# Kernel optimization log

Measured on AMD Instinct MI355X. Metric: run time of the kernel, lower is better.

The kernel has to match this reference:

```python
import jax, jax.numpy as jnp
import numpy as np

N = 50000      # nodes
E = 800000     # edges (avg degree 16)
IN = 128       # in_feats
HID = 32       # hidden_feats per head
H = 4          # num_heads
NEG_SLOPE = 0.2


def setup_inputs() -> dict:
    key = jax.random.key(0)
    ks = jax.random.split(key, 13)
    x = jax.random.normal(ks[0], (N, IN), jnp.float32)
    src = jax.random.randint(ks[1], (E,), 0, N, jnp.int32)
    dst = jax.random.randint(ks[2], (E,), 0, N, jnp.int32)

    def lin(k, fi, fo):
        return jax.random.normal(k, (fi, fo), jnp.float32) * (1.0 / np.sqrt(fi))

    # conv1: IN -> H*HID
    W1 = lin(ks[3], IN, H * HID)
    al1 = jax.random.normal(ks[4], (H, HID), jnp.float32) * 0.1
    ar1 = jax.random.normal(ks[5], (H, HID), jnp.float32) * 0.1
    b1 = jnp.zeros((H, HID), jnp.float32)
    # conv2: H*HID -> H*HID
    W2 = lin(ks[6], H * HID, H * HID)
    al2 = jax.random.normal(ks[7], (H, HID), jnp.float32) * 0.1
    ar2 = jax.random.normal(ks[8], (H, HID), jnp.float32) * 0.1
    b2 = jnp.zeros((H, HID), jnp.float32)
    # fc: HID -> 1
    fcW = lin(ks[9], HID, 1)
    fcb = jnp.zeros((1,), jnp.float32)
    return {"x": x, "src": src, "dst": dst,
            "W1": W1, "al1": al1, "ar1": ar1, "b1": b1,
            "W2": W2, "al2": al2, "ar2": ar2, "b2": b2,
            "fcW": fcW, "fcb": fcb}


def gat_conv(x, src, dst, W, al, ar, b):
    # x: [N, F_in] -> feat: [N, H, HID]
    feat = (x @ W).reshape(N, H, HID)
    el = jnp.sum(feat * al, axis=-1)            # [N, H]
    er = jnp.sum(feat * ar, axis=-1)            # [N, H]
    e = jax.nn.leaky_relu(el[src] + er[dst], NEG_SLOPE)  # [E, H]
    # segment softmax over incoming edges of each dst node
    m = jax.ops.segment_max(e, dst, num_segments=N)      # [N, H]
    ex = jnp.exp(e - m[dst])                              # [E, H]
    denom = jax.ops.segment_sum(ex, dst, num_segments=N)  # [N, H]
    alpha = ex / denom[dst]                                # [E, H]
    msg = feat[src] * alpha[:, :, None]                    # [E, H, HID]
    out = jax.ops.segment_sum(msg, dst, num_segments=N)   # [N, H, HID]
    return out + b[None, :, :]


def reference(x, src, dst, W1, al1, ar1, b1, W2, al2, ar2, b2, fcW, fcb):
    h = gat_conv(x, src, dst, W1, al1, ar1, b1).reshape(N, H * HID)
    h = jax.nn.relu(h)
    # dropout(0.5) is identity in eval mode
    h = gat_conv(h, src, dst, W2, al2, ar2, b2).mean(axis=1)  # [N, HID]
    return h @ fcW + fcb                                       # [N, 1]
```

## Files before the change

### kernel.cpp

```cpp
#include <hip/hip_runtime.h>
#include <hip/hip_fp16.h>

#define LEAK 0.2f
#define CAP 64
#define CS 16

static __device__ inline int swz(int c, int j) {
    int qb = j >> 3, r = j & 7;
    return c * 144 + qb * 8 + (qb >> 2) * 4 + r;
}
static __device__ inline unsigned q4(float4 v, float is) {
    int x0 = __float2int_rn(v.x * is) + 128; x0 = min(max(x0, 0), 255);
    int x1 = __float2int_rn(v.y * is) + 128; x1 = min(max(x1, 0), 255);
    int x2 = __float2int_rn(v.z * is) + 128; x2 = min(max(x2, 0), 255);
    int x3 = __float2int_rn(v.w * is) + 128; x3 = min(max(x3, 0), 255);
    return (unsigned)x0 | ((unsigned)x1 << 8) | ((unsigned)x2 << 16) | ((unsigned)x3 << 24);
}

__global__ __launch_bounds__(256, 4) void k1(
    const float* __restrict__ X, const float* __restrict__ W,
    const float* __restrict__ al, const float* __restrict__ ar,
    float2* __restrict__ elsc2, float* __restrict__ er_nh,
    unsigned* __restrict__ fq8,
    int* __restrict__ cnt,
    const float* __restrict__ W2, const float* __restrict__ al2,
    const float* __restrict__ ar2, const float* __restrict__ fcW,
    const float* __restrict__ b2, float* __restrict__ WfT,
    float* __restrict__ bc, int N, int ntiles, int zb) {
    __shared__ float sW[32 * 128];
    __shared__ float sXT[32 * 128];
    const int b = blockIdx.x;
    const int t = threadIdx.x;

    if (b >= ntiles) {
        int bb = b - ntiles;
        if (bb < zb) {
            int i = bb * 256 + t;
            if (i < N * (CS / 4)) {
                ((int4*)cnt)[i] = make_int4(0, 0, 0, 0);
            }
        } else {
            int idx = (bb - zb) * 256 + t;
            if (idx < 1536) {
                int c = idx >> 7, k = idx & 127;
                int h = c & 3, sel = c >> 2;
                const float* vec = (sel == 0) ? (al2 + 32 * h)
                                 : (sel == 1) ? (ar2 + 32 * h) : fcW;
                float s = 0.f;
#pragma unroll 8
                for (int m = 0; m < 32; m++) s += W2[k * 128 + 32 * h + m] * vec[m];
                WfT[c * 128 + k] = s;
            } else if (idx < 1540) {
                int h = idx - 1536;
                float s = 0.f;
                for (int m = 0; m < 32; m++) s += b2[h * 32 + m] * fcW[m];
                bc[h] = s;
            }
        }
        return;
    }

    const int r0 = b * 128;
    const int tx = t & 15;
    const int ty = t >> 4;
    const float4* X4 = (const float4*)X;
    const float4* W4 = (const float4*)W;
    float4* sW4 = (float4*)sW;
    const float4* sXT4 = (const float4*)sXT;

    float4 acc[8][2];
#pragma unroll
    for (int r = 0; r < 8; r++) {
        acc[r][0] = make_float4(0.f, 0.f, 0.f, 0.f);
        acc[r][1] = make_float4(0.f, 0.f, 0.f, 0.f);
    }
    for (int ks = 0; ks < 4; ++ks) {
        if (ks) __syncthreads();
#pragma unroll
        for (int i = 0; i < 4; i++) {
            int idx = i * 256 + t;
            sW4[idx] = W4[1024 * ks + idx];
        }
#pragma unroll
        for (int i = 0; i < 4; i++) {
            int idx = i * 256 + t;
            int row = idx >> 3;
            int kq = idx & 7;
            float4 v = make_float4(0.f, 0.f, 0.f, 0.f);
            if (r0 + row < N) v = X4[(size_t)(r0 + row) * 32 + ks * 8 + kq];
            int sc = (((row >> 2) ^ kq)) * 4 + (row & 3);
            sXT[(4 * kq + 0) * 128 + sc] = v.x;
            sXT[(4 * kq + 1) * 128 + sc] = v.y;
            sXT[(4 * kq + 2) * 128 + sc] = v.z;
            sXT[(4 * kq + 3) * 128 + sc] = v.w;
        }
        __syncthreads();
#pragma unroll 4
        for (int k = 0; k < 32; k++) {
            float4 w0 = sW4[k * 32 + tx];
            float4 w1 = sW4[k * 32 + 16 + tx];
            float4 x0 = sXT4[k * 32 + (ty ^ (k >> 2))];
            float4 x1 = sXT4[k * 32 + ((16 + ty) ^ (k >> 2))];
            float xs[8] = {x0.x, x0.y, x0.z, x0.w, x1.x, x1.y, x1.z, x1.w};
#pragma unroll
            for (int r = 0; r < 8; r++) {
                acc[r][0].x += xs[r] * w0.x; acc[r][0].y += xs[r] * w0.y;
                acc[r][0].z += xs[r] * w0.z; acc[r][0].w += xs[r] * w0.w;
                acc[r][1].x += xs[r] * w1.x; acc[r][1].y += xs[r] * w1.y;
                acc[r][1].z += xs[r] * w1.z; acc[r][1].w += xs[r] * w1.w;
            }
        }
    }
    const float4* al4p = (const float4*)al;
    const float4* ar4p = (const float4*)ar;
    float4 alA = al4p[tx], alB = al4p[16 + tx];
    float4 arA = ar4p[tx], arB = ar4p[16 + tx];
#pragma unroll
    for (int r = 0; r < 8; r++) {
        int lrow = (r < 4) ? (ty * 4 + r) : (64 + ty * 4 + (r - 4));
        int row = r0 + lrow;
        bool ok = row < N;
        float4 a0 = acc[r][0], a1 = acc[r][1];
        float m = fmaxf(fmaxf(fmaxf(fabsf(a0.x), fabsf(a0.y)),
                              fmaxf(fabsf(a0.z), fabsf(a0.w))),
                        fmaxf(fmaxf(fabsf(a1.x), fabsf(a1.y)),
                              fmaxf(fabsf(a1.z), fabsf(a1.w))));
#pragma unroll
        for (int off = 1; off < 16; off <<= 1) m = fmaxf(m, __shfl_xor(m, off));
        float scale = m * (1.f / 127.f);
        float is = (m > 0.f) ? (127.f / m) : 0.f;
        if (ok) {
            fq8[(size_t)row * 32 + tx] = q4(a0, is);
            fq8[(size_t)row * 32 + 16 + tx] = q4(a1, is);
        }
        float elA = a0.x * alA.x + a0.y * alA.y + a0.z * alA.z + a0.w * alA.w;
        float erA = a0.x * arA.x + a0.y * arA.y + a0.z * arA.z + a0.w * arA.w;
        float elB = a1.x * alB.x + a1.y * alB.y + a1.z * alB.z + a1.w * alB.w;
        float erB = a1.x * arB.x + a1.y * arB.y + a1.z * arB.z + a1.w * arB.w;
#pragma unroll
        for (int off = 1; off < 8; off <<= 1) {
            elA += __shfl_xor(elA, off); erA += __shfl_xor(erA, off);
            elB += __shfl_xor(elB, off); erB += __shfl_xor(erB, off);
        }
        if (ok && tx == 0) {
            elsc2[row * 4 + 0] = make_float2(elA, scale);
            elsc2[row * 4 + 2] = make_float2(elB, scale);
            er_nh[row * 4 + 0] = erA;
            er_nh[row * 4 + 2] = erB;
        }
        if (ok && tx == 8) {
            elsc2[row * 4 + 1] = make_float2(elA, scale);
            elsc2[row * 4 + 3] = make_float2(elB, scale);
            er_nh[row * 4 + 1] = erA;
            er_nh[row * 4 + 3] = erB;
        }
    }
}

__global__ __launch_bounds__(256) void k_ell(
    const int* __restrict__ src, const int* __restrict__ dst,
    int* __restrict__ cnt, unsigned short* __restrict__ ell,
    int E, int N, int R) {
    const int part = blockIdx.x & 7;
    const int rank = blockIdx.x >> 3;
    const int S = (N + 7) >> 3;
    const int lo = part * S;
    const int hi = (lo + S < N) ? (lo + S) : N;
    const int per = (E + R - 1) / R;
    const int e0 = rank * per;
    const int e1 = (e0 + per < E) ? (e0 + per) : E;
    for (int e = e0 + threadIdx.x; e < e1; e += 256) {
        int d = dst[e];
        if (d >= lo && d < hi) {
            int s = src[e];
            int pos = atomicAdd(&cnt[d * CS], 1);
            if (pos < CAP) ell[(size_t)d * CAP + pos] = (unsigned short)s;
        }
    }
}

__global__ __launch_bounds__(256) void k_agg1P(
    const unsigned* __restrict__ fq8, const float2* __restrict__ elsc2,
    const float* __restrict__ er_nh, const unsigned short* __restrict__ ell,
    const int* __restrict__ cnt, const float* __restrict__ b1,
    const float* __restrict__ WfT, float2* __restrict__ Pag,
    float* __restrict__ er2, int N) {
    __shared__ float sWf[12 * 144];
    for (int i = threadIdx.x; i < 1536; i += 256)
        sWf[swz(i >> 7, i & 127)] = WfT[i];
    __syncthreads();
    const int wave = threadIdx.x >> 6, lane = threadIdx.x & 63;
    const int nsub = lane >> 4, q = lane & 15, h = q >> 2;
    const int wbase = q * 8 + (q >> 2) * 4;
    const uint2* fq2 = (const uint2*)fq8;

    const int n = blockIdx.x * 16 + wave * 4 + nsub;
    const bool nok = n < N;
    const int nc = nok ? n : (N - 1);
    int deg = nok ? cnt[n * CS] : 0; if (deg > CAP) deg = CAP;
    float er = nok ? er_nh[n * 4 + h] : 0.f;
    const unsigned short* row = ell + (size_t)nc * CAP;

    int dm = deg;
    dm = max(dm, __shfl_xor(dm, 16));
    dm = max(dm, __shfl_xor(dm, 32));

    float acc[8] = {0.f, 0.f, 0.f, 0.f, 0.f, 0.f, 0.f, 0.f};
    float den = 0.f, wss = 0.f;
    for (int jt = 0; jt < dm; jt += 16) {
        int s_all = (jt + q < CAP) ? (int)row[jt + q] : 0;
        int lim = dm - jt; if (lim > 16) lim = 16;
        for (int u = 0; u < lim; u += 8) {
            int sv[8]; float2 esv[8]; uint2 fv[8];
#pragma unroll
            for (int v = 0; v < 8; v++) {
                int jj = jt + u + v;
                int s = __shfl(s_all, (lane & 48) | ((u + v) & 15));
                sv[v] = (jj < deg) ? s : 0;
            }
#pragma unroll
            for (int v = 0; v < 8; v++) esv[v] = elsc2[sv[v] * 4 + h];
#pragma unroll
            for (int v = 0; v < 8; v++) fv[v] = fq2[(size_t)sv[v] * 16 + q];
#pragma unroll
            for (int v = 0; v < 8; v++) {
                int jj = jt + u + v;
                bool valid = jj < deg;
                float e = esv[v].x + er;
                e = fmaxf(e, LEAK * e);
                float w = valid ? __expf(e) : 0.f;
                float ws = w * esv[v].y;
                unsigned ua = fv[v].x, ub = fv[v].y;
                acc[0] += ws * (float)(ua & 0xff);
                acc[1] += ws * (float)((ua >> 8) & 0xff);
                acc[2] += ws * (float)((ua >> 16) & 0xff);
                acc[3] += ws * (float)(ua >> 24);
                acc[4] += ws * (float)(ub & 0xff);
                acc[5] += ws * (float)((ub >> 8) & 0xff);
                acc[6] += ws * (float)((ub >> 16) & 0xff);
                acc[7] += ws * (float)(ub >> 24);
                den += w; wss += ws;
            }
        }
    }
    float inv = (den > 0.f) ? (1.f / den) : 0.f;
    float off128 = 128.f * wss;
    float4 b1a = ((const float4*)b1)[q * 2];
    float4 b1b = ((const float4*)b1)[q * 2 + 1];
    float hv[8];
    hv[0] = fmaxf((acc[0] - off128) * inv + b1a.x, 0.f);
    hv[1] = fmaxf((acc[1] - off128) * inv + b1a.y, 0.f);
    hv[2] = fmaxf((acc[2] - off128) * inv + b1a.z, 0.f);
    hv[3] = fmaxf((acc[3] - off128) * inv + b1a.w, 0.f);
    hv[4] = fmaxf((acc[4] - off128) * inv + b1b.x, 0.f);
    hv[5] = fmaxf((acc[5] - off128) * inv + b1b.y, 0.f);
    hv[6] = fmaxf((acc[6] - off128) * inv + b1b.z, 0.f);
    hv[7] = fmaxf((acc[7] - off128) * inv + b1b.w, 0.f);
    float p[12];
#pragma unroll
    for (int c = 0; c < 12; c++) {
        const float* wr = sWf + c * 144 + wbase;
        float4 wa = *(const float4*)wr;
        float4 wb = *(const float4*)(wr + 4);
        p[c] = hv[0] * wa.x + hv[1] * wa.y + hv[2] * wa.z + hv[3] * wa.w
             + hv[4] * wb.x + hv[5] * wb.y + hv[6] * wb.z + hv[7] * wb.w;
    }
#pragma unroll
    for (int off = 1; off < 16; off <<= 1) {
#pragma unroll
        for (int c = 0; c < 12; c++) p[c] += __shfl_xor(p[c], off);
    }
    if (nok) {
        if (q < 4) Pag[(size_t)n * 4 + q] = make_float2(p[q], p[8 + q]);
        else if (q < 8) er2[(size_t)n * 4 + (q - 4)] = p[q];
    }
}

__global__ __launch_bounds__(256) void k_agg2(
    const float2* __restrict__ Pag, const float* __restrict__ er2,
    const unsigned short* __restrict__ ell, const int* __restrict__ cnt,
    const float* __restrict__ bc, const float* __restrict__ fcb,
    float* __restrict__ out, int N) {
    int idx = blockIdx.x * 256 + threadIdx.x;
    int n = idx >> 2, h = idx & 3;
    if (n >= N) return;
    int deg = cnt[n * CS]; if (deg > CAP) deg = CAP;
    float er = er2[(size_t)n * 4 + h];
    const unsigned short* row = ell + (size_t)n * CAP;
    float num = 0.f, den = 0.f;
    int j = 0, d8 = deg & ~7;
    for (; j < d8; j += 8) {
        ushort4 sa = *(const ushort4*)(row + j);
        ushort4 sb = *(const ushort4*)(row + j + 4);
        int sv[8] = {sa.x, sa.y, sa.z, sa.w, sb.x, sb.y, sb.z, sb.w};
        float2 g[8];
#pragma unroll
        for (int v = 0; v < 8; v++) g[v] = Pag[(size_t)sv[v] * 4 + h];
#pragma unroll
        for (int v = 0; v < 8; v++) {
            float e = g[v].x + er; e = fmaxf(e, LEAK * e);
            float w = __expf(e);
            num += w * g[v].y; den += w;
        }
    }
    for (; j < deg; ++j) {
        int s = row[j];
        float2 gg = Pag[(size_t)s * 4 + h];
        float e = gg.x + er; e = fmaxf(e, LEAK * e);
        float w = __expf(e);
        num += w * gg.y; den += w;
    }
    float r = (den > 0.f) ? (num / den) : 0.f;
    r += bc[h];
    r += __shfl_xor(r, 1);
    r += __shfl_xor(r, 2);
    if (h == 0) out[n] = 0.25f * r + fcb[0];
}

extern "C" void kernel_launch(void* const* d_in, const int* in_sizes, int n_in,
                              void* d_out, int out_size, void* d_ws, size_t ws_size,
                              hipStream_t stream) {
    const float* x   = (const float*)d_in[0];
    const int* src   = (const int*)d_in[1];
    const int* dst   = (const int*)d_in[2];
    const float* W1  = (const float*)d_in[3];
    const float* al1 = (const float*)d_in[4];
    const float* ar1 = (const float*)d_in[5];
    const float* b1  = (const float*)d_in[6];
    const float* W2  = (const float*)d_in[7];
    const float* al2 = (const float*)d_in[8];
    const float* ar2 = (const float*)d_in[9];
    const float* b2  = (const float*)d_in[10];
    const float* fcW = (const float*)d_in[11];
    const float* fcb = (const float*)d_in[12];
    float* out = (float*)d_out;

    const int N = in_sizes[0] / 128;
    const int E = in_sizes[1];

    char* w = (char*)d_ws;
    size_t off = 0;
    auto alloc = [&](size_t bytes) {
        void* p = w + off;
        off = (off + bytes + 255) & ~(size_t)255;
        return p;
    };
    unsigned* fq8  = (unsigned*)alloc((size_t)N * 32 * 4);
    float2* elsc2  = (float2*)alloc((size_t)N * 4 * 8);
    float* er_nh   = (float*)alloc((size_t)N * 4 * 4);
    float2* Pag    = (float2*)alloc((size_t)N * 4 * 8);
    float* er2     = (float*)alloc((size_t)N * 4 * 4);
    float* WfT     = (float*)alloc((size_t)(12 * 128 + 4) * 4);
    float* bc      = WfT + 12 * 128;
    int* cnt       = (int*)alloc((size_t)N * CS * 4);
    unsigned short* ell = (unsigned short*)alloc((size_t)N * CAP * 2);

    const int zb = (N * (CS / 4) + 255) / 256;
    const int ntiles = (N + 127) / 128;
    const int R = 256;

    k1<<<ntiles + zb + 8, 256, 0, stream>>>(
        x, W1, al1, ar1, elsc2, er_nh, fq8,
        cnt, W2, al2, ar2, fcW, b2, WfT, bc, N, ntiles, zb);
    k_ell<<<8 * R, 256, 0, stream>>>(src, dst, cnt, ell, E, N, R);
    k_agg1P<<<(N + 15) / 16, 256, 0, stream>>>(
        fq8, elsc2, er_nh, ell, cnt, b1, WfT, Pag, er2, N);
    k_agg2<<<(N * 4 + 255) / 256, 256, 0, stream>>>(
        Pag, er2, ell, cnt, bc, fcb, out, N);
}
```

Baseline: 200.5 us.

## Fuse ELL build into GEMM kernel and move init work to separate kernel

Moves the cnt zeroing and the W2/fcW folding into a new small kernel k0. The ELL-construction blocks are merged into the first-layer GEMM kernel as extra blocks so edge bucketing runs concurrently with the feature projection. The GEMM tile shrinks from 128 to 64 rows per block, halving accumulators and shared memory, which gives more blocks to mix with the atomic-heavy ELL blocks. The cost is an extra launch for k0 and less register-level reuse per GEMM block.

```diff
diff --git a/kernel.cpp b/kernel.cpp
--- a/kernel.cpp
+++ b/kernel.cpp
@@ -17,50 +17,72 @@
     return (unsigned)x0 | ((unsigned)x1 << 8) | ((unsigned)x2 << 16) | ((unsigned)x3 << 24);
 }
 
-__global__ __launch_bounds__(256, 4) void k1(
+__global__ __launch_bounds__(256) void k0(
+    int* __restrict__ cnt,
+    const float* __restrict__ W2, const float* __restrict__ al2,
+    const float* __restrict__ ar2, const float* __restrict__ fcW,
+    const float* __restrict__ b2, float* __restrict__ WfT,
+    float* __restrict__ bc, int N, int zb) {
+    const int b = blockIdx.x;
+    const int t = threadIdx.x;
+    if (b < zb) {
+        int i = b * 256 + t;
+        if (i < N * (CS / 4)) ((int4*)cnt)[i] = make_int4(0, 0, 0, 0);
+        return;
+    }
+    int idx = (b - zb) * 256 + t;
+    if (idx < 1536) {
+        int c = idx >> 7, k = idx & 127;
+        int h = c & 3, sel = c >> 2;
+        const float* vec = (sel == 0) ? (al2 + 32 * h)
+                         : (sel == 1) ? (ar2 + 32 * h) : fcW;
+        float s = 0.f;
+#pragma unroll 8
+        for (int m = 0; m < 32; m++) s += W2[k * 128 + 32 * h + m] * vec[m];
+        WfT[c * 128 + k] = s;
+    } else if (idx < 1540) {
+        int h = idx - 1536;
+        float s = 0.f;
+        for (int m = 0; m < 32; m++) s += b2[h * 32 + m] * fcW[m];
+        bc[h] = s;
+    }
+}
+
+__global__ __launch_bounds__(256, 4) void k1f(
     const float* __restrict__ X, const float* __restrict__ W,
     const float* __restrict__ al, const float* __restrict__ ar,
     float2* __restrict__ elsc2, float* __restrict__ er_nh,
     unsigned* __restrict__ fq8,
-    int* __restrict__ cnt,
-    const float* __restrict__ W2, const float* __restrict__ al2,
-    const float* __restrict__ ar2, const float* __restrict__ fcW,
-    const float* __restrict__ b2, float* __restrict__ WfT,
-    float* __restrict__ bc, int N, int ntiles, int zb) {
+    const int* __restrict__ src, const int* __restrict__ dst,
+    int* __restrict__ cnt, unsigned short* __restrict__ ell,
+    int N, int E, int gtiles, int R) {
     __shared__ float sW[32 * 128];
-    __shared__ float sXT[32 * 128];
+    __shared__ float sXT[32 * 64];
     const int b = blockIdx.x;
     const int t = threadIdx.x;
 
-    if (b >= ntiles) {
-        int bb = b - ntiles;
-        if (bb < zb) {
-            int i = bb * 256 + t;
-            if (i < N * (CS / 4)) {
-                ((int4*)cnt)[i] = make_int4(0, 0, 0, 0);
+    if (b >= gtiles) {
+        const int bb = b - gtiles;
+        const int part = bb & 7;
+        const int rank = bb >> 3;
+        const int S = (N + 7) >> 3;
+        const int lo = part * S;
+        const int hi = (lo + S < N) ? (lo + S) : N;
+        const int per = (E + R - 1) / R;
+        const int e0 = rank * per;
+        const int e1 = (e0 + per < E) ? (e0 + per) : E;
+        for (int e = e0 + t; e < e1; e += 256) {
+            int d = dst[e];
+            if (d >= lo && d < hi) {
+                int s = src[e];
+                int pos = atomicAdd(&cnt[d * CS], 1);
+                if (pos < CAP) ell[(size_t)d * CAP + pos] = (unsigned short)s;
             }
-        } else {
-            int idx = (bb - zb) * 256 + t;
-            if (idx < 1536) {
-                int c = idx >> 7, k = idx & 127;
-                int h = c & 3, sel = c >> 2;
-                const float* vec = (sel == 0) ? (al2 + 32 * h)
-                                 : (sel == 1) ? (ar2 + 32 * h) : fcW;
-                float s = 0.f;
-#pragma unroll 8
-                for (int m = 0; m < 32; m++) s += W2[k * 128 + 32 * h + m] * vec[m];
-                WfT[c * 128 + k] = s;
-            } else if (idx < 1540) {
-                int h = idx - 1536;
-                float s = 0.f;
-                for (int m = 0; m < 32; m++) s += b2[h * 32 + m] * fcW[m];
-                bc[h] = s;
-            }
         }
         return;
     }
 
-    const int r0 = b * 128;
+    const int r0 = b * 64;
     const int tx = t & 15;
     const int ty = t >> 4;
     const float4* X4 = (const float4*)X;
@@ -68,9 +90,9 @@
     float4* sW4 = (float4*)sW;
     const float4* sXT4 = (const float4*)sXT;
 
-    float4 acc[8][2];
-#pragma unroll
-    for (int r = 0; r < 8; r++) {
+    float4 acc[4][2];
+#pragma unroll
+    for (int r = 0; r < 4; r++) {
         acc[r][0] = make_float4(0.f, 0.f, 0.f, 0.f);
         acc[r][1] = make_float4(0.f, 0.f, 0.f, 0.f);
     }
@@ -82,28 +104,27 @@
             sW4[idx] = W4[1024 * ks + idx];
         }
 #pragma unroll
-        for (int i = 0; i < 4; i++) {
+        for (int i = 0; i < 2; i++) {
             int idx = i * 256 + t;
             int row = idx >> 3;
             int kq = idx & 7;
             float4 v = make_float4(0.f, 0.f, 0.f, 0.f);
             if (r0 + row < N) v = X4[(size_t)(r0 + row) * 32 + ks * 8 + kq];
-            int sc = (((row >> 2) ^ kq)) * 4 + (row & 3);
-            sXT[(4 * kq + 0) * 128 + sc] = v.x;
-            sXT[(4 * kq + 1) * 128 + sc] = v.y;
-            sXT[(4 * kq + 2) * 128 + sc] = v.z;
-            sXT[(4 * kq + 3) * 128 + sc] = v.w;
+            int sc = ((row >> 2) ^ kq) * 4 + (row & 3);
+            sXT[(4 * kq + 0) * 64 + sc] = v.x;
+            sXT[(4 * kq + 1) * 64 + sc] = v.y;
+            sXT[(4 * kq + 2) * 64 + sc] = v.z;
+            sXT[(4 * kq + 3) * 64 + sc] = v.w;
         }
         __syncthreads();
 #pragma unroll 4
         for (int k = 0; k < 32; k++) {
             float4 w0 = sW4[k * 32 + tx];
             float4 w1 = sW4[k * 32 + 16 + tx];
-            float4 x0 = sXT4[k * 32 + (ty ^ (k >> 2))];
-            float4 x1 = sXT4[k * 32 + ((16 + ty) ^ (k >> 2))];
-            float xs[8] = {x0.x, x0.y, x0.z, x0.w, x1.x, x1.y, x1.z, x1.w};
-#pragma unroll
-            for (int r = 0; r < 8; r++) {
+            float4 x0 = sXT4[k * 16 + (ty ^ (k >> 2))];
+            float xs[4] = {x0.x, x0.y, x0.z, x0.w};
+#pragma unroll
+            for (int r = 0; r < 4; r++) {
                 acc[r][0].x += xs[r] * w0.x; acc[r][0].y += xs[r] * w0.y;
                 acc[r][0].z += xs[r] * w0.z; acc[r][0].w += xs[r] * w0.w;
                 acc[r][1].x += xs[r] * w1.x; acc[r][1].y += xs[r] * w1.y;
@@ -116,9 +137,8 @@
     float4 alA = al4p[tx], alB = al4p[16 + tx];
     float4 arA = ar4p[tx], arB = ar4p[16 + tx];
 #pragma unroll
-    for (int r = 0; r < 8; r++) {
-        int lrow = (r < 4) ? (ty * 4 + r) : (64 + ty * 4 + (r - 4));
-        int row = r0 + lrow;
+    for (int r = 0; r < 4; r++) {
+        int row = r0 + ty * 4 + r;
         bool ok = row < N;
         float4 a0 = acc[r][0], a1 = acc[r][1];
         float m = fmaxf(fmaxf(fmaxf(fabsf(a0.x), fabsf(a0.y)),
@@ -153,28 +173,6 @@
             elsc2[row * 4 + 3] = make_float2(elB, scale);
             er_nh[row * 4 + 1] = erA;
             er_nh[row * 4 + 3] = erB;
-        }
-    }
-}
-
-__global__ __launch_bounds__(256) void k_ell(
-    const int* __restrict__ src, const int* __restrict__ dst,
-    int* __restrict__ cnt, unsigned short* __restrict__ ell,
-    int E, int N, int R) {
-    const int part = blockIdx.x & 7;
-    const int rank = blockIdx.x >> 3;
-    const int S = (N + 7) >> 3;
-    const int lo = part * S;
-    const int hi = (lo + S < N) ? (lo + S) : N;
-    const int per = (E + R - 1) / R;
-    const int e0 = rank * per;
-    const int e1 = (e0 + per < E) ? (e0 + per) : E;
-    for (int e = e0 + threadIdx.x; e < e1; e += 256) {
-        int d = dst[e];
-        if (d >= lo && d < hi) {
-            int s = src[e];
-            int pos = atomicAdd(&cnt[d * CS], 1);
-            if (pos < CAP) ell[(size_t)d * CAP + pos] = (unsigned short)s;
         }
     }
 }
@@ -356,13 +354,14 @@
     unsigned short* ell = (unsigned short*)alloc((size_t)N * CAP * 2);
 
     const int zb = (N * (CS / 4) + 255) / 256;
-    const int ntiles = (N + 127) / 128;
+    const int gtiles = (N + 63) / 64;
     const int R = 256;
 
-    k1<<<ntiles + zb + 8, 256, 0, stream>>>(
+    k0<<<zb + 7, 256, 0, stream>>>(
+        cnt, W2, al2, ar2, fcW, b2, WfT, bc, N, zb);
+    k1f<<<gtiles + 8 * R, 256, 0, stream>>>(
         x, W1, al1, ar1, elsc2, er_nh, fq8,
-        cnt, W2, al2, ar2, fcW, b2, WfT, bc, N, ntiles, zb);
-    k_ell<<<8 * R, 256, 0, stream>>>(src, dst, cnt, ell, E, N, R);
+        src, dst, cnt, ell, N, E, gtiles, R);
     k_agg1P<<<(N + 15) / 16, 256, 0, stream>>>(
         fq8, elsc2, er_nh, ell, cnt, b1, WfT, Pag, er2, N);
     k_agg2<<<(N * 4 + 255) / 256, 256, 0, stream>>>(
```

Result: faster. 189.9 us (-5.3%).
